# Optimization experiments

Measured on AMD Instinct MI355X. Metric: run time of the kernel, lower is better.

Reference implementation:

```python
import jax, jax.numpy as jnp
import numpy as np

PS = 4          # patch size
C = 3           # channels
VOCAB = 512
D = 256         # embed dim
PD = PS * PS * C  # 48 patch dim


def _gelu(x):
    return jax.nn.gelu(x, approximate=False)  # torch nn.GELU default = exact erf


def setup_inputs() -> dict:
    key = jax.random.key(0)
    ks = jax.random.split(key, 16)
    frames = jax.random.uniform(ks[0], (32, 256, 256, 3), jnp.float32) * 255.0

    def lin(kw, kb, fan_in, fan_out):
        bound = 1.0 / np.sqrt(fan_in)
        w = jax.random.uniform(kw, (fan_out, fan_in), jnp.float32, -bound, bound)
        b = jax.random.uniform(kb, (fan_out,), jnp.float32, -bound, bound)
        return w, b

    enc_w1, enc_b1 = lin(ks[1], ks[2], PD, D)
    enc_w2, enc_b2 = lin(ks[3], ks[4], D, D)
    enc_w3, enc_b3 = lin(ks[5], ks[6], D, D)
    dec_w1, dec_b1 = lin(ks[7], ks[8], D, D)
    dec_w2, dec_b2 = lin(ks[9], ks[10], D, D)
    dec_w3, dec_b3 = lin(ks[11], ks[12], D, PD)
    codebook = jax.random.normal(ks[13], (VOCAB, D), jnp.float32) * 0.1
    return {
        'frames': frames,
        'enc_w1': enc_w1, 'enc_b1': enc_b1,
        'enc_w2': enc_w2, 'enc_b2': enc_b2,
        'enc_w3': enc_w3, 'enc_b3': enc_b3,
        'codebook': codebook,
        'dec_w1': dec_w1, 'dec_b1': dec_b1,
        'dec_w2': dec_w2, 'dec_b2': dec_b2,
        'dec_w3': dec_w3, 'dec_b3': dec_b3,
    }


def _patchify(x):  # [B,H,W,C] -> [B, N, ps*ps*C]
    B, H, W, Ch = x.shape
    h, w = H // PS, W // PS
    x = x.reshape(B, h, PS, w, PS, Ch).transpose(0, 1, 3, 2, 4, 5)
    return x.reshape(B, h * w, PS * PS * Ch)


def _unpatchify(p):  # [B, N, ps*ps*C] -> [B,H,W,C]
    B, N, _ = p.shape
    h = w = int(np.sqrt(N))
    p = p.reshape(B, h, w, PS, PS, C).transpose(0, 1, 3, 2, 4, 5)
    return p.reshape(B, h * PS, w * PS, C)


def reference(frames, enc_w1, enc_b1, enc_w2, enc_b2, enc_w3, enc_b3,
              codebook, dec_w1, dec_b1, dec_w2, dec_b2, dec_w3, dec_b3):
    x = frames / 255.0 * 2.0 - 1.0
    patches = _patchify(x)  # [B,N,48]
    # encoder MLP
    z = _gelu(patches @ enc_w1.T + enc_b1)
    z = _gelu(z @ enc_w2.T + enc_b2)
    z_e = z @ enc_w3.T + enc_b3  # [B,N,D]
    # nearest-codebook lookup (squared L2; argmin equals cdist argmin)
    d2 = (jnp.sum(z_e * z_e, -1, keepdims=True)
          - 2.0 * jnp.einsum('bnd,vd->bnv', z_e, codebook)
          + jnp.sum(codebook * codebook, -1))  # [B,N,V]
    tokens = jnp.argmin(d2, axis=-1)  # [B,N] int
    z_q = codebook[tokens]  # [B,N,D]
    z_q_st = z_e + jax.lax.stop_gradient(z_q - z_e)
    # decoder MLP
    y = _gelu(z_q_st @ dec_w1.T + dec_b1)
    y = _gelu(y @ dec_w2.T + dec_b2)
    y = y @ dec_w3.T + dec_b3  # [B,N,48]
    recon = _unpatchify(y)
    target = frames / 255.0 * 2.0 - 1.0
    recon_loss = jnp.mean((recon - target) ** 2)
    commitment_loss = jnp.mean((z_e - jax.lax.stop_gradient(z_q)) ** 2)
    codebook_loss = jnp.mean((z_q - jax.lax.stop_gradient(z_e)) ** 2)
    return recon, tokens, recon_loss, commitment_loss, codebook_loss
```

## Files before the change

kernel.cpp:

```cpp
#include <hip/hip_runtime.h>
#include <hip/hip_bf16.h>
#include <math.h>
#include <float.h>
#include <limits.h>

#define T_ROWS 131072

typedef __attribute__((ext_vector_type(8))) short short8;
typedef __attribute__((ext_vector_type(4))) float f32x4;

__device__ __forceinline__ float gelu_f(float x){
    return 0.5f * x * (1.0f + erff(x * 0.7071067811865475f));
}
__device__ __forceinline__ float bf2f(ushort u){
    union { unsigned int i; float f; } v; v.i = ((unsigned int)u) << 16; return v.f;
}
__device__ __forceinline__ ushort f2bf(float f){
    union { float f; unsigned int i; } v; v.f = f;
    unsigned int i = v.i;
    unsigned int r = (i + 0x7fffu + ((i >> 16) & 1u)) >> 16;
    return (ushort)r;
}
__device__ __forceinline__ void split3(float x, ushort &u0, ushort &u1, ushort &u2){
    union { float f; unsigned int i; } v; v.f = x;
    u0 = (ushort)(v.i >> 16);
    union { unsigned int i; float f; } h0; h0.i = ((unsigned int)u0) << 16;
    float r = x - h0.f;
    union { float f; unsigned int i; } vr; vr.f = r;
    u1 = (ushort)(vr.i >> 16);
    union { unsigned int i; float f; } h1; h1.i = ((unsigned int)u1) << 16;
    float r2 = r - h1.f;
    union { float f; unsigned int i; } v2; v2.f = r2;
    u2 = (ushort)(v2.i >> 16);
}

__global__ __launch_bounds__(256) void prep_kernel(
    const float* __restrict__ w2, const float* __restrict__ w3,
    const float* __restrict__ d1, const float* __restrict__ d2,
    const float* __restrict__ w1, const float* __restrict__ b1,
    const float* __restrict__ cb,
    ushort* __restrict__ w2s0, ushort* __restrict__ w2s1, ushort* __restrict__ w2s2,
    ushort* __restrict__ w3s0, ushort* __restrict__ w3s1, ushort* __restrict__ w3s2,
    ushort* __restrict__ w1b, ushort* __restrict__ w2b,
    float* __restrict__ cn, ushort* __restrict__ cbb,
    ushort* __restrict__ cbs0, ushort* __restrict__ cbs1, ushort* __restrict__ cbs2,
    ushort* __restrict__ w1p0, ushort* __restrict__ w1p1, ushort* __restrict__ w1p2,
    float* __restrict__ bias2)
{
    const int blk = blockIdx.x, tid = threadIdx.x;
    if (blk < 64){
        const int i = (blk*256 + tid)*4;
        float4 a = *(const float4*)(w2 + i);
        ushort4 s0, s1, s2;
        split3(a.x, s0.x, s1.x, s2.x); split3(a.y, s0.y, s1.y, s2.y);
        split3(a.z, s0.z, s1.z, s2.z); split3(a.w, s0.w, s1.w, s2.w);
        *(ushort4*)(w2s0+i)=s0; *(ushort4*)(w2s1+i)=s1; *(ushort4*)(w2s2+i)=s2;
        float4 b = *(const float4*)(w3 + i);
        split3(b.x, s0.x, s1.x, s2.x); split3(b.y, s0.y, s1.y, s2.y);
        split3(b.z, s0.z, s1.z, s2.z); split3(b.w, s0.w, s1.w, s2.w);
        *(ushort4*)(w3s0+i)=s0; *(ushort4*)(w3s1+i)=s1; *(ushort4*)(w3s2+i)=s2;
        float4 c = *(const float4*)(d1 + i);
        ushort4 u; u.x=f2bf(c.x); u.y=f2bf(c.y); u.z=f2bf(c.z); u.w=f2bf(c.w);
        *(ushort4*)(w1b+i) = u;
        float4 d = *(const float4*)(d2 + i);
        u.x=f2bf(d.x); u.y=f2bf(d.y); u.z=f2bf(d.z); u.w=f2bf(d.w);
        *(ushort4*)(w2b+i) = u;
    } else if (blk < 192){
        const int lane = tid & 63;
        const int code = (blk-64)*4 + (tid >> 6);
        float4 v = ((const float4*)(cb + (size_t)code*256))[lane];
        size_t off = (size_t)code*256 + lane*4;
        ushort4 u; u.x=f2bf(v.x); u.y=f2bf(v.y); u.z=f2bf(v.z); u.w=f2bf(v.w);
        *(ushort4*)(cbb + off) = u;
        ushort4 s0, s1, s2;
        split3(v.x, s0.x, s1.x, s2.x); split3(v.y, s0.y, s1.y, s2.y);
        split3(v.z, s0.z, s1.z, s2.z); split3(v.w, s0.w, s1.w, s2.w);
        *(ushort4*)(cbs0 + off) = s0;
        *(ushort4*)(cbs1 + off) = s1;
        *(ushort4*)(cbs2 + off) = s2;
        float s = v.x*v.x + v.y*v.y + v.z*v.z + v.w*v.w;
        #pragma unroll
        for (int m=1; m<64; m<<=1) s += __shfl_xor(s, m);
        if (lane == 0) cn[code] = s;
    } else if (blk < 208){
        const int idx = (blk-192)*256 + tid;
        const int n = idx >> 4, k = (idx & 15)*4;
        ushort4 s0 = {0,0,0,0}, s1 = {0,0,0,0}, s2 = {0,0,0,0};
        if (k < 48){
            float4 v = *(const float4*)(w1 + n*48 + k);
            split3(v.x, s0.x, s1.x, s2.x); split3(v.y, s0.y, s1.y, s2.y);
            split3(v.z, s0.z, s1.z, s2.z); split3(v.w, s0.w, s1.w, s2.w);
        }
        *(ushort4*)(w1p0 + n*64 + k) = s0;
        *(ushort4*)(w1p1 + n*64 + k) = s1;
        *(ushort4*)(w1p2 + n*64 + k) = s2;
    } else {
        float s = 0.0f;
        for (int k=0;k<48;++k) s += w1[tid*48 + k];
        bias2[tid] = b1[tid] - s;
    }
}

template<int KTOT, bool GELU, int LOADER, bool SCALE>
__global__ __launch_bounds__(256, 3) void split6_gemm(
    const float* __restrict__ Ain,
    const float* __restrict__ frames,
    const ushort* __restrict__ W0, const ushort* __restrict__ W1,
    const ushort* __restrict__ W2,
    const float* __restrict__ bias,
    float* __restrict__ Cout)
{
    __shared__ __align__(16) ushort Al[3][64][40];
    __shared__ __align__(16) ushort Wl[256][40];

    const int tid = threadIdx.x;
    const int m0 = blockIdx.x * 64;
    const int arow = tid >> 2, q = tid & 3;
    const int lane = tid & 63;
    const int w = tid >> 6;
    const int lr = lane & 15, lg = lane >> 4;

    const float* asrc = nullptr;
    int pbase = 0;
    if constexpr (LOADER == 0){
        asrc = Ain + (size_t)(m0 + arow)*KTOT + q*8;
    } else {
        int p = m0 + arow;
        int b = p >> 12, nl = p & 4095, hh = nl >> 6, ww = nl & 63;
        pbase = ((b*256 + hh*4)*256 + ww*4)*3;
    }
    const ushort* wsrc  = W0 + (size_t)tid*KTOT;
    const ushort* w1frag = W1 + (size_t)(w*64 + lr)*KTOT + lg*8;
    const ushort* w2frag = W2 + (size_t)(w*64 + lr)*KTOT + lg*8;

    f32x4 acc[4][4];
    #pragma unroll
    for (int mi=0;mi<4;++mi)
        #pragma unroll
        for (int ni=0;ni<4;++ni)
            acc[mi][ni] = (f32x4){0.f,0.f,0.f,0.f};

    for (int k0=0; k0<KTOT; k0+=32){
        float x[8];
        if constexpr (LOADER == 0){
            *(float4*)&x[0] = *(const float4*)(asrc + k0);
            *(float4*)&x[4] = *(const float4*)(asrc + k0 + 4);
        } else {
            #pragma unroll
            for (int j=0;j<2;++j){
                int kk = k0 + q*8 + j*4;
                float4 v = {0.f,0.f,0.f,0.f};
                if (kk < 48){
                    int ph = kk/12, rem = kk - ph*12;
                    v = *(const float4*)(frames + pbase + ph*768 + rem);
                }
                x[j*4+0]=v.x; x[j*4+1]=v.y; x[j*4+2]=v.z; x[j*4+3]=v.w;
            }
        }
        ushort t0[8], t1[8], t2[8];
        #pragma unroll
        for (int e=0;e<8;++e) split3(x[e], t0[e], t1[e], t2[e]);
        *(uint4*)&Al[0][arow][q*8] = *(const uint4*)t0;
        *(uint4*)&Al[1][arow][q*8] = *(const uint4*)t1;
        *(uint4*)&Al[2][arow][q*8] = *(const uint4*)t2;
        *(uint4*)&Wl[tid][0]  = *(const uint4*)(wsrc + k0);
        *(uint4*)&Wl[tid][8]  = *(const uint4*)(wsrc + k0 + 8);
        *(uint4*)&Wl[tid][16] = *(const uint4*)(wsrc + k0 + 16);
        *(uint4*)&Wl[tid][24] = *(const uint4*)(wsrc + k0 + 24);
        short8 b1v[4], b2v[4];
        #pragma unroll
        for (int ni=0;ni<4;++ni){
            b1v[ni] = *(const short8*)(w1frag + (size_t)ni*16*KTOT + k0);
            b2v[ni] = *(const short8*)(w2frag + (size_t)ni*16*KTOT + k0);
        }
        __syncthreads();

        short8 b0v[4];
        #pragma unroll
        for (int ni=0;ni<4;++ni)
            b0v[ni] = *(const short8*)&Wl[w*64 + ni*16 + lr][lg*8];
        #pragma unroll
        for (int mi=0;mi<4;++mi){
            short8 a0 = *(const short8*)&Al[0][mi*16 + lr][lg*8];
            short8 a1 = *(const short8*)&Al[1][mi*16 + lr][lg*8];
            short8 a2 = *(const short8*)&Al[2][mi*16 + lr][lg*8];
            #pragma unroll
            for (int ni=0;ni<4;++ni)
                acc[mi][ni] = __builtin_amdgcn_mfma_f32_16x16x32_bf16(a0, b0v[ni], acc[mi][ni], 0,0,0);
            #pragma unroll
            for (int ni=0;ni<4;++ni)
                acc[mi][ni] = __builtin_amdgcn_mfma_f32_16x16x32_bf16(a0, b1v[ni], acc[mi][ni], 0,0,0);
            #pragma unroll
            for (int ni=0;ni<4;++ni)
                acc[mi][ni] = __builtin_amdgcn_mfma_f32_16x16x32_bf16(a1, b0v[ni], acc[mi][ni], 0,0,0);
            #pragma unroll
            for (int ni=0;ni<4;++ni)
                acc[mi][ni] = __builtin_amdgcn_mfma_f32_16x16x32_bf16(a0, b2v[ni], acc[mi][ni], 0,0,0);
            #pragma unroll
            for (int ni=0;ni<4;++ni)
                acc[mi][ni] = __builtin_amdgcn_mfma_f32_16x16x32_bf16(a1, b1v[ni], acc[mi][ni], 0,0,0);
            #pragma unroll
            for (int ni=0;ni<4;++ni)
                acc[mi][ni] = __builtin_amdgcn_mfma_f32_16x16x32_bf16(a2, b0v[ni], acc[mi][ni], 0,0,0);
        }
        __syncthreads();
    }

    const float alpha = 2.0f/255.0f;
    float bn[4];
    #pragma unroll
    for (int ni=0;ni<4;++ni) bn[ni] = bias[w*64 + ni*16 + lr];
    #pragma unroll
    for (int mi=0;mi<4;++mi)
        #pragma unroll
        for (int ni=0;ni<4;++ni)
            #pragma unroll
            for (int r=0;r<4;++r){
                int row = m0 + mi*16 + lg*4 + r;
                float v;
                if (SCALE) v = fmaf(alpha, acc[mi][ni][r], bn[ni]);
                else       v = acc[mi][ni][r] + bn[ni];
                if (GELU) v = gelu_f(v);
                Cout[(size_t)row*256 + w*64 + ni*16 + lr] = v;
            }
}

#define INSERT1(dv, iv) do { \
    float _d = (dv); int _i = (iv); \
    if (_d < bd || (_d == bd && _i < bi)){ bd = _d; bi = _i; } \
} while(0)

__global__ __launch_bounds__(256, 3) void tokens_split6(
    const float* __restrict__ Zf,
    const ushort* __restrict__ C0, const ushort* __restrict__ C1,
    const ushort* __restrict__ C2,
    const float* __restrict__ cn,
    float2* __restrict__ partials,
    float* __restrict__ zz_out)
{
    __shared__ __align__(16) ushort Al[3][128][40];
    __shared__ __align__(16) ushort Wl[2][128][40];
    __shared__ float2 ptop[128][2];

    const int tid = threadIdx.x;
    const int m0 = blockIdx.x * 128;
    const int n0 = blockIdx.y * 128;
    const int srow = tid >> 1, shalf = (tid & 1) * 16;
    const int lane = tid & 63;
    const int w = tid >> 6;
    const int wm = (w >> 1) * 64, wn = (w & 1) * 64;
    const int lr = lane & 15, lg = lane >> 4;

    const float*  asrc = Zf + (size_t)(m0 + srow)*256 + shalf;
    const ushort* ws0  = C0 + (size_t)(n0 + srow)*256 + shalf;
    const ushort* ws1  = C1 + (size_t)(n0 + srow)*256 + shalf;
    const ushort* c2frag = C2 + (size_t)(n0 + wn + lr)*256 + lg*8;

    f32x4 acc[4][4];
    #pragma unroll
    for (int mi=0;mi<4;++mi)
        #pragma unroll
        for (int ni=0;ni<4;++ni)
            acc[mi][ni] = (f32x4){0.f,0.f,0.f,0.f};

    float zzp = 0.0f;

    for (int k0=0; k0<256; k0+=32){
        float x[16];
        *(float4*)&x[0]  = *(const float4*)(asrc + k0);
        *(float4*)&x[4]  = *(const float4*)(asrc + k0 + 4);
        *(float4*)&x[8]  = *(const float4*)(asrc + k0 + 8);
        *(float4*)&x[12] = *(const float4*)(asrc + k0 + 12);
        ushort t0[16], t1[16], t2[16];
        #pragma unroll
        for (int e=0;e<16;++e){
            split3(x[e], t0[e], t1[e], t2[e]);
            zzp = fmaf(x[e], x[e], zzp);
        }
        *(uint4*)&Al[0][srow][shalf]   = *(const uint4*)&t0[0];
        *(uint4*)&Al[0][srow][shalf+8] = *(const uint4*)&t0[8];
        *(uint4*)&Al[1][srow][shalf]   = *(const uint4*)&t1[0];
        *(uint4*)&Al[1][srow][shalf+8] = *(const uint4*)&t1[8];
        *(uint4*)&Al[2][srow][shalf]   = *(const uint4*)&t2[0];
        *(uint4*)&Al[2][srow][shalf+8] = *(const uint4*)&t2[8];
        *(uint4*)&Wl[0][srow][shalf]   = *(const uint4*)(ws0 + k0);
        *(uint4*)&Wl[0][srow][shalf+8] = *(const uint4*)(ws0 + k0 + 8);
        *(uint4*)&Wl[1][srow][shalf]   = *(const uint4*)(ws1 + k0);
        *(uint4*)&Wl[1][srow][shalf+8] = *(const uint4*)(ws1 + k0 + 8);
        short8 b2[4];
        #pragma unroll
        for (int ni=0;ni<4;++ni)
            b2[ni] = *(const short8*)(c2frag + (size_t)ni*16*256 + k0);
        __syncthreads();

        short8 b0[4], b1[4];
        #pragma unroll
        for (int ni=0;ni<4;++ni){
            b0[ni] = *(const short8*)&Wl[0][wn + ni*16 + lr][lg*8];
            b1[ni] = *(const short8*)&Wl[1][wn + ni*16 + lr][lg*8];
        }
        #pragma unroll
        for (int mi=0;mi<4;++mi){
            short8 a0 = *(const short8*)&Al[0][wm + mi*16 + lr][lg*8];
            short8 a1 = *(const short8*)&Al[1][wm + mi*16 + lr][lg*8];
            short8 a2 = *(const short8*)&Al[2][wm + mi*16 + lr][lg*8];
            #pragma unroll
            for (int ni=0;ni<4;++ni)
                acc[mi][ni] = __builtin_amdgcn_mfma_f32_16x16x32_bf16(a0, b0[ni], acc[mi][ni], 0,0,0);
            #pragma unroll
            for (int ni=0;ni<4;++ni)
                acc[mi][ni] = __builtin_amdgcn_mfma_f32_16x16x32_bf16(a0, b1[ni], acc[mi][ni], 0,0,0);
            #pragma unroll
            for (int ni=0;ni<4;++ni)
                acc[mi][ni] = __builtin_amdgcn_mfma_f32_16x16x32_bf16(a1, b0[ni], acc[mi][ni], 0,0,0);
            #pragma unroll
            for (int ni=0;ni<4;++ni)
                acc[mi][ni] = __builtin_amdgcn_mfma_f32_16x16x32_bf16(a0, b2[ni], acc[mi][ni], 0,0,0);
            #pragma unroll
            for (int ni=0;ni<4;++ni)
                acc[mi][ni] = __builtin_amdgcn_mfma_f32_16x16x32_bf16(a1, b1[ni], acc[mi][ni], 0,0,0);
            #pragma unroll
            for (int ni=0;ni<4;++ni)
                acc[mi][ni] = __builtin_amdgcn_mfma_f32_16x16x32_bf16(a2, b0[ni], acc[mi][ni], 0,0,0);
        }
        __syncthreads();
    }

    {
        float other = __shfl_xor(zzp, 1);
        if (blockIdx.y == 0 && (tid & 1) == 0)
            zz_out[m0 + srow] = zzp + other;
    }

    float cnl[4];
    #pragma unroll
    for (int ni=0;ni<4;++ni) cnl[ni] = cn[n0 + wn + ni*16 + lr];

    #pragma unroll
    for (int mi=0;mi<4;++mi)
        #pragma unroll
        for (int r=0;r<4;++r){
            float bd = FLT_MAX; int bi = INT_MAX;
            #pragma unroll
            for (int ni=0;ni<4;++ni){
                float d = cnl[ni] - 2.0f*acc[mi][ni][r];
                int col = n0 + wn + ni*16 + lr;
                INSERT1(d, col);
            }
            #pragma unroll
            for (int m=1; m<16; m<<=1){
                float od = __shfl_xor(bd, m);
                int   oi = __shfl_xor(bi, m);
                INSERT1(od, oi);
            }
            if (lr == 0)
                ptop[wm + mi*16 + lg*4 + r][w & 1] = make_float2(bd, (float)bi);
        }
    __syncthreads();
    if (tid < 128){
        float2 hA = ptop[tid][0], hB = ptop[tid][1];
        int   gA = (int)hA.y, gB = (int)hB.y;
        bool takeB = (hB.x < hA.x) || (hB.x == hA.x && gB < gA);
        partials[(size_t)(m0 + tid)*4 + blockIdx.y] = takeB ? hB : hA;
    }
}

__global__ __launch_bounds__(256) void token_reduce(
    const float* __restrict__ zz_out, const float2* __restrict__ partials,
    float* __restrict__ tokf, float* __restrict__ loss)
{
    const int tid = threadIdx.x;
    const int row = blockIdx.x*256 + tid;
    float2 p0 = partials[(size_t)row*4 + 0];
    float2 p1 = partials[(size_t)row*4 + 1];
    float2 p2 = partials[(size_t)row*4 + 2];
    float2 p3 = partials[(size_t)row*4 + 3];
    float d = p0.x; int g = (int)p0.y;
    if (p1.x < d || (p1.x == d && (int)p1.y < g)){ d = p1.x; g = (int)p1.y; }
    if (p2.x < d || (p2.x == d && (int)p2.y < g)){ d = p2.x; g = (int)p2.y; }
    if (p3.x < d || (p3.x == d && (int)p3.y < g)){ d = p3.x; g = (int)p3.y; }
    tokf[row] = (float)g;
    float cs = zz_out[row] + d;
    #pragma unroll
    for (int m=1; m<64; m<<=1) cs += __shfl_xor(cs, m);
    __shared__ float wsum[4];
    const int lane = tid & 63, w = tid >> 6;
    if (lane == 0) wsum[w] = cs;
    __syncthreads();
    if (tid == 0) atomicAdd(loss + 1, wsum[0]+wsum[1]+wsum[2]+wsum[3]);
}

__global__ __launch_bounds__(256) void mfma_gemm(
    const ushort* __restrict__ Abf,
    const ushort* __restrict__ Wbf,
    const float* __restrict__ bias,
    ushort* __restrict__ Ybf)
{
    __shared__ __align__(16) ushort Al[128][40];
    __shared__ __align__(16) ushort Wl[128][40];

    const int tid = threadIdx.x;
    const int m0 = blockIdx.x * 128;
    const int n0 = blockIdx.y * 128;
    const int srow = tid >> 1, shalf = (tid & 1) * 16;
    const int lane = tid & 63;
    const int w = tid >> 6;
    const int wm = (w >> 1) * 64, wn = (w & 1) * 64;
    const int lr = lane & 15, lg = lane >> 4;

    const ushort* asrc = Abf + (size_t)(m0 + srow)*256 + shalf;
    const ushort* wsrc = Wbf + (size_t)(n0 + srow)*256 + shalf;

    f32x4 acc[4][4];
    #pragma unroll
    for (int mi=0;mi<4;++mi)
        #pragma unroll
        for (int ni=0;ni<4;++ni)
            acc[mi][ni] = (f32x4){0.f,0.f,0.f,0.f};

    for (int k0=0; k0<256; k0+=32){
        *(uint4*)&Al[srow][shalf]   = *(const uint4*)(asrc + k0);
        *(uint4*)&Al[srow][shalf+8] = *(const uint4*)(asrc + k0 + 8);
        *(uint4*)&Wl[srow][shalf]   = *(const uint4*)(wsrc + k0);
        *(uint4*)&Wl[srow][shalf+8] = *(const uint4*)(wsrc + k0 + 8);
        __syncthreads();

        short8 af[4], bfr[4];
        #pragma unroll
        for (int mi=0;mi<4;++mi)
            af[mi] = *(const short8*)&Al[wm + mi*16 + lr][lg*8];
        #pragma unroll
        for (int ni=0;ni<4;++ni)
            bfr[ni] = *(const short8*)&Wl[wn + ni*16 + lr][lg*8];
        #pragma unroll
        for (int mi=0;mi<4;++mi)
            #pragma unroll
            for (int ni=0;ni<4;++ni)
                acc[mi][ni] = __builtin_amdgcn_mfma_f32_16x16x32_bf16(
                    af[mi], bfr[ni], acc[mi][ni], 0, 0, 0);
        __syncthreads();
    }

    float bn[4];
    #pragma unroll
    for (int ni=0;ni<4;++ni) bn[ni] = bias[n0 + wn + ni*16 + lr];
    #pragma unroll
    for (int mi=0;mi<4;++mi)
        #pragma unroll
        for (int ni=0;ni<4;++ni)
            #pragma unroll
            for (int r=0;r<4;++r){
                int row = m0 + wm + mi*16 + lg*4 + r;
                float v = acc[mi][ni][r] + bn[ni];
                v = gelu_f(v);
                Ybf[(size_t)row*256 + n0 + wn + ni*16 + lr] = f2bf(v);
            }
}

__global__ __launch_bounds__(256) void dec3_table(
    const ushort* __restrict__ Ain, const float* __restrict__ W,
    const float* __restrict__ bias, float* __restrict__ Rt)
{
    __shared__ __align__(16) ushort Al[256][40];
    __shared__ __align__(16) ushort Wl[48][40];

    const int tid = threadIdx.x;
    const int m0 = blockIdx.x * 256;
    const int lane = tid & 63;
    const int w = tid >> 6;
    const int lr = lane & 15, lg = lane >> 4;

    const ushort* asrc = Ain + (size_t)(m0 + tid)*256;

    f32x4 acc[4][3];
    #pragma unroll
    for (int mi=0;mi<4;++mi)
        #pragma unroll
        for (int ni=0;ni<3;++ni)
            acc[mi][ni] = (f32x4){0.f,0.f,0.f,0.f};

    for (int k0=0; k0<256; k0+=32){
        *(uint4*)&Al[tid][0]  = *(const uint4*)(asrc + k0);
        *(uint4*)&Al[tid][8]  = *(const uint4*)(asrc + k0 + 8);
        *(uint4*)&Al[tid][16] = *(const uint4*)(asrc + k0 + 16);
        *(uint4*)&Al[tid][24] = *(const uint4*)(asrc + k0 + 24);
        if (tid < 96){
            const int wrow = tid >> 1, wh = (tid & 1)*16;
            const float* wp = W + (size_t)wrow*256 + k0 + wh;
            float4 f0 = *(const float4*)(wp);
            float4 f1 = *(const float4*)(wp+4);
            float4 f2 = *(const float4*)(wp+8);
            float4 f3 = *(const float4*)(wp+12);
            ushort t[16];
            t[0]=f2bf(f0.x); t[1]=f2bf(f0.y); t[2]=f2bf(f0.z); t[3]=f2bf(f0.w);
            t[4]=f2bf(f1.x); t[5]=f2bf(f1.y); t[6]=f2bf(f1.z); t[7]=f2bf(f1.w);
            t[8]=f2bf(f2.x); t[9]=f2bf(f2.y); t[10]=f2bf(f2.z); t[11]=f2bf(f2.w);
            t[12]=f2bf(f3.x); t[13]=f2bf(f3.y); t[14]=f2bf(f3.z); t[15]=f2bf(f3.w);
            *(uint4*)&Wl[wrow][wh]   = *(const uint4*)&t[0];
            *(uint4*)&Wl[wrow][wh+8] = *(const uint4*)&t[8];
        }
        __syncthreads();

        short8 bfr[3];
        #pragma unroll
        for (int ni=0;ni<3;++ni)
            bfr[ni] = *(const short8*)&Wl[ni*16 + lr][lg*8];
        #pragma unroll
        for (int mi=0;mi<4;++mi){
            short8 af = *(const short8*)&Al[w*64 + mi*16 + lr][lg*8];
            #pragma unroll
            for (int ni=0;ni<3;++ni)
                acc[mi][ni] = __builtin_amdgcn_mfma_f32_16x16x32_bf16(
                    af, bfr[ni], acc[mi][ni], 0, 0, 0);
        }
        __syncthreads();
    }

    #pragma unroll
    for (int ni=0;ni<3;++ni){
        const int col = ni*16 + lr;
        const float bn = bias[col];
        #pragma unroll
        for (int mi=0;mi<4;++mi)
            #pragma unroll
            for (int r=0;r<4;++r){
                int row = m0 + w*64 + mi*16 + lg*4 + r;
                Rt[row*48 + col] = acc[mi][ni][r] + bn;
            }
    }
}

__global__ __launch_bounds__(256) void gather_recon(
    const float* __restrict__ Rt, const float* __restrict__ tokf,
    const float* __restrict__ frames, float* __restrict__ recon,
    float* __restrict__ loss)
{
    const int tid = threadIdx.x;
    const int idx = blockIdx.x*256 + tid;
    const int p = idx >> 2, ph = idx & 3;
    const int g = (int)tokf[p];
    int b = p >> 12, nl = p & 4095, hh = nl >> 6, ww = nl & 63;
    size_t base = (size_t)(((b*256 + hh*4 + ph)*256 + ww*4)*3);
    const float* rp = Rt + g*48 + ph*12;
    const float sc = 2.0f/255.0f;
    float ls = 0.0f;
    #pragma unroll
    for (int j=0;j<3;++j){
        float4 y = *(const float4*)(rp + j*4);
        float4 f = *(const float4*)(frames + base + j*4);
        float t0=f.x*sc-1.0f, t1=f.y*sc-1.0f, t2=f.z*sc-1.0f, t3=f.w*sc-1.0f;
        float d0=y.x-t0, d1=y.y-t1, d2=y.z-t2, d3=y.w-t3;
        ls += d0*d0 + d1*d1 + d2*d2 + d3*d3;
        *(float4*)(recon + base + j*4) = y;
    }
    #pragma unroll
    for (int off=32; off>0; off>>=1) ls += __shfl_down(ls, off);
    __shared__ float wsum[4];
    int lane = tid & 63, w = tid >> 6;
    if (lane == 0) wsum[w] = ls;
    __syncthreads();
    if (tid == 0) atomicAdd(loss + 0, wsum[0]+wsum[1]+wsum[2]+wsum[3]);
}

__global__ void finalize_kernel(float* __restrict__ loss){
    if (threadIdx.x == 0 && blockIdx.x == 0){
        loss[0] = loss[0] * (1.0f/6291456.0f);
        float c = loss[1] * (1.0f/33554432.0f);
        loss[1] = c;
        loss[2] = c;
    }
}

extern "C" void kernel_launch(void* const* d_in, const int* in_sizes, int n_in,
                              void* d_out, int out_size, void* d_ws, size_t ws_size,
                              hipStream_t stream)
{
    (void)in_sizes; (void)n_in; (void)out_size; (void)ws_size;
    const float* frames   = (const float*)d_in[0];
    const float* enc_w1   = (const float*)d_in[1];
    const float* enc_b1   = (const float*)d_in[2];
    const float* enc_w2   = (const float*)d_in[3];
    const float* enc_b2   = (const float*)d_in[4];
    const float* enc_w3   = (const float*)d_in[5];
    const float* enc_b3   = (const float*)d_in[6];
    const float* codebook = (const float*)d_in[7];
    const float* dec_w1   = (const float*)d_in[8];
    const float* dec_b1   = (const float*)d_in[9];
    const float* dec_w2   = (const float*)d_in[10];
    const float* dec_b2   = (const float*)d_in[11];
    const float* dec_w3   = (const float*)d_in[12];
    const float* dec_b3   = (const float*)d_in[13];

    float* P = (float*)d_ws;
    float* Q = P + (size_t)33554432;
    float2* partials = (float2*)(Q + 18000000);
    ushort* L1 = (ushort*)P;
    ushort* L2 = (ushort*)(P + 65536);
    float*  Rt = P + 131072;

    float* recon = (float*)d_out;
    float* tokf  = recon + 6291456;
    float* loss  = tokf + 131072;
    float*  cn   = recon;
    ushort* cbb  = (ushort*)(recon + 512);
    ushort* w1b  = (ushort*)(recon + 66048);
    ushort* w2b  = (ushort*)(recon + 98816);
    ushort* w2s0 = (ushort*)(recon + 131584);
    ushort* w2s1 = (ushort*)(recon + 164352);
    ushort* w2s2 = (ushort*)(recon + 197120);
    ushort* w3s0 = (ushort*)(recon + 229888);
    ushort* w3s1 = (ushort*)(recon + 262656);
    ushort* w3s2 = (ushort*)(recon + 295424);
    ushort* cbs0 = (ushort*)(recon + 328192);
    ushort* cbs1 = (ushort*)(recon + 393728);
    ushort* cbs2 = (ushort*)(recon + 459264);
    float*  zzb  = recon + 524800;
    ushort* w1p0 = (ushort*)(recon + 655872);
    ushort* w1p1 = (ushort*)(recon + 664064);
    ushort* w1p2 = (ushort*)(recon + 672256);
    float*  bias2 = recon + 680448;

    hipMemsetAsync(loss, 0, 3*sizeof(float), stream);

    dim3 blk(256);
    prep_kernel<<<dim3(209), blk, 0, stream>>>(enc_w2, enc_w3, dec_w1, dec_w2,
        enc_w1, enc_b1, codebook,
        w2s0, w2s1, w2s2, w3s0, w3s1, w3s2, w1b, w2b,
        cn, cbb, cbs0, cbs1, cbs2, w1p0, w1p1, w1p2, bias2);
    split6_gemm<64,  true, 1, true ><<<dim3(T_ROWS/64), blk, 0, stream>>>(nullptr, frames, w1p0, w1p1, w1p2, bias2, P);
    split6_gemm<256, true, 0, false><<<dim3(T_ROWS/64), blk, 0, stream>>>(P, nullptr, w2s0, w2s1, w2s2, enc_b2, Q);
    split6_gemm<256, false,0, false><<<dim3(T_ROWS/64), blk, 0, stream>>>(Q, nullptr, w3s0, w3s1, w3s2, enc_b3, P);
    tokens_split6<<<dim3(T_ROWS/128, 4), blk, 0, stream>>>(P, cbs0, cbs1, cbs2, cn, partials, zzb);
    token_reduce<<<dim3(T_ROWS/256), blk, 0, stream>>>(zzb, partials, tokf, loss);
    mfma_gemm<<<dim3(4, 2), blk, 0, stream>>>(cbb, w1b, dec_b1, L1);
    mfma_gemm<<<dim3(4, 2), blk, 0, stream>>>(L1, w2b, dec_b2, L2);
    dec3_table<<<dim3(2), blk, 0, stream>>>(L2, dec_w3, dec_b3, Rt);
    gather_recon<<<dim3(T_ROWS*4/256), blk, 0, stream>>>(Rt, tokf, frames, recon, loss);
    finalize_kernel<<<dim3(1), dim3(64), 0, stream>>>(loss);
}
```

Measured before the change: 597.7 us.

## Emit pre-split bf16 z_e and row norms from enc3 GEMM epilogue for token search

The third encoder GEMM now writes z_e directly as three bf16 split planes and computes per-row squared norms in its epilogue. A new token-search kernel reads those planes instead of re-splitting fp32 z_e in each of the four codebook column blocks. This removes repeated split work and the fp32 reads in the token kernel. In exchange it writes three ushort planes (same byte count as fp32 times 1.5) and needs a larger workspace, with fallback to the old path if the workspace is too small.

```diff
diff --git a/kernel.cpp b/kernel.cpp
--- a/kernel.cpp
+++ b/kernel.cpp
@@ -225,6 +225,117 @@
             }
 }
 
+__global__ __launch_bounds__(256, 3) void split6_zout(
+    const float* __restrict__ Ain,
+    const ushort* __restrict__ W0, const ushort* __restrict__ W1,
+    const ushort* __restrict__ W2,
+    const float* __restrict__ bias,
+    ushort* __restrict__ zb0, ushort* __restrict__ zb1, ushort* __restrict__ zb2,
+    float* __restrict__ zz_out)
+{
+    __shared__ __align__(16) ushort Al[3][64][40];
+    __shared__ __align__(16) ushort Wl[256][40];
+    __shared__ float zs[64][4];
+
+    const int tid = threadIdx.x;
+    const int m0 = blockIdx.x * 64;
+    const int arow = tid >> 2, q = tid & 3;
+    const int lane = tid & 63;
+    const int w = tid >> 6;
+    const int lr = lane & 15, lg = lane >> 4;
+
+    const float* asrc = Ain + (size_t)(m0 + arow)*256 + q*8;
+    const ushort* wsrc  = W0 + (size_t)tid*256;
+    const ushort* w1frag = W1 + (size_t)(w*64 + lr)*256 + lg*8;
+    const ushort* w2frag = W2 + (size_t)(w*64 + lr)*256 + lg*8;
+
+    f32x4 acc[4][4];
+    #pragma unroll
+    for (int mi=0;mi<4;++mi)
+        #pragma unroll
+        for (int ni=0;ni<4;++ni)
+            acc[mi][ni] = (f32x4){0.f,0.f,0.f,0.f};
+
+    for (int k0=0; k0<256; k0+=32){
+        float x[8];
+        *(float4*)&x[0] = *(const float4*)(asrc + k0);
+        *(float4*)&x[4] = *(const float4*)(asrc + k0 + 4);
+        ushort t0[8], t1[8], t2[8];
+        #pragma unroll
+        for (int e=0;e<8;++e) split3(x[e], t0[e], t1[e], t2[e]);
+        *(uint4*)&Al[0][arow][q*8] = *(const uint4*)t0;
+        *(uint4*)&Al[1][arow][q*8] = *(const uint4*)t1;
+        *(uint4*)&Al[2][arow][q*8] = *(const uint4*)t2;
+        *(uint4*)&Wl[tid][0]  = *(const uint4*)(wsrc + k0);
+        *(uint4*)&Wl[tid][8]  = *(const uint4*)(wsrc + k0 + 8);
+        *(uint4*)&Wl[tid][16] = *(const uint4*)(wsrc + k0 + 16);
+        *(uint4*)&Wl[tid][24] = *(const uint4*)(wsrc + k0 + 24);
+        short8 b1v[4], b2v[4];
+        #pragma unroll
+        for (int ni=0;ni<4;++ni){
+            b1v[ni] = *(const short8*)(w1frag + (size_t)ni*16*256 + k0);
+            b2v[ni] = *(const short8*)(w2frag + (size_t)ni*16*256 + k0);
+        }
+        __syncthreads();
+
+        short8 b0v[4];
+        #pragma unroll
+        for (int ni=0;ni<4;++ni)
+            b0v[ni] = *(const short8*)&Wl[w*64 + ni*16 + lr][lg*8];
+        #pragma unroll
+        for (int mi=0;mi<4;++mi){
+            short8 a0 = *(const short8*)&Al[0][mi*16 + lr][lg*8];
+            short8 a1 = *(const short8*)&Al[1][mi*16 + lr][lg*8];
+            short8 a2 = *(const short8*)&Al[2][mi*16 + lr][lg*8];
+            #pragma unroll
+            for (int ni=0;ni<4;++ni)
+                acc[mi][ni] = __builtin_amdgcn_mfma_f32_16x16x32_bf16(a0, b0v[ni], acc[mi][ni], 0,0,0);
+            #pragma unroll
+            for (int ni=0;ni<4;++ni)
+                acc[mi][ni] = __builtin_amdgcn_mfma_f32_16x16x32_bf16(a0, b1v[ni], acc[mi][ni], 0,0,0);
+            #pragma unroll
+            for (int ni=0;ni<4;++ni)
+                acc[mi][ni] = __builtin_amdgcn_mfma_f32_16x16x32_bf16(a1, b0v[ni], acc[mi][ni], 0,0,0);
+            #pragma unroll
+            for (int ni=0;ni<4;++ni)
+                acc[mi][ni] = __builtin_amdgcn_mfma_f32_16x16x32_bf16(a0, b2v[ni], acc[mi][ni], 0,0,0);
+            #pragma unroll
+            for (int ni=0;ni<4;++ni)
+                acc[mi][ni] = __builtin_amdgcn_mfma_f32_16x16x32_bf16(a1, b1v[ni], acc[mi][ni], 0,0,0);
+            #pragma unroll
+            for (int ni=0;ni<4;++ni)
+                acc[mi][ni] = __builtin_amdgcn_mfma_f32_16x16x32_bf16(a2, b0v[ni], acc[mi][ni], 0,0,0);
+        }
+        __syncthreads();
+    }
+
+    float bn[4];
+    #pragma unroll
+    for (int ni=0;ni<4;++ni) bn[ni] = bias[w*64 + ni*16 + lr];
+    #pragma unroll
+    for (int mi=0;mi<4;++mi)
+        #pragma unroll
+        for (int r=0;r<4;++r){
+            int row = m0 + mi*16 + lg*4 + r;
+            float p = 0.0f;
+            #pragma unroll
+            for (int ni=0;ni<4;++ni){
+                float v = acc[mi][ni][r] + bn[ni];
+                p = fmaf(v, v, p);
+                ushort s0, s1, s2;
+                split3(v, s0, s1, s2);
+                size_t off = (size_t)row*256 + w*64 + ni*16 + lr;
+                zb0[off] = s0; zb1[off] = s1; zb2[off] = s2;
+            }
+            p += __shfl_xor(p, 1); p += __shfl_xor(p, 2);
+            p += __shfl_xor(p, 4); p += __shfl_xor(p, 8);
+            if (lr == 0) zs[mi*16 + lg*4 + r][w] = p;
+        }
+    __syncthreads();
+    if (tid < 64)
+        zz_out[m0 + tid] = zs[tid][0] + zs[tid][1] + zs[tid][2] + zs[tid][3];
+}
+
 #define INSERT1(dv, iv) do { \
     float _d = (dv); int _i = (iv); \
     if (_d < bd || (_d == bd && _i < bi)){ bd = _d; bi = _i; } \
@@ -330,6 +441,122 @@
         float other = __shfl_xor(zzp, 1);
         if (blockIdx.y == 0 && (tid & 1) == 0)
             zz_out[m0 + srow] = zzp + other;
+    }
+
+    float cnl[4];
+    #pragma unroll
+    for (int ni=0;ni<4;++ni) cnl[ni] = cn[n0 + wn + ni*16 + lr];
+
+    #pragma unroll
+    for (int mi=0;mi<4;++mi)
+        #pragma unroll
+        for (int r=0;r<4;++r){
+            float bd = FLT_MAX; int bi = INT_MAX;
+            #pragma unroll
+            for (int ni=0;ni<4;++ni){
+                float d = cnl[ni] - 2.0f*acc[mi][ni][r];
+                int col = n0 + wn + ni*16 + lr;
+                INSERT1(d, col);
+            }
+            #pragma unroll
+            for (int m=1; m<16; m<<=1){
+                float od = __shfl_xor(bd, m);
+                int   oi = __shfl_xor(bi, m);
+                INSERT1(od, oi);
+            }
+            if (lr == 0)
+                ptop[wm + mi*16 + lg*4 + r][w & 1] = make_float2(bd, (float)bi);
+        }
+    __syncthreads();
+    if (tid < 128){
+        float2 hA = ptop[tid][0], hB = ptop[tid][1];
+        int   gA = (int)hA.y, gB = (int)hB.y;
+        bool takeB = (hB.x < hA.x) || (hB.x == hA.x && gB < gA);
+        partials[(size_t)(m0 + tid)*4 + blockIdx.y] = takeB ? hB : hA;
+    }
+}
+
+__global__ __launch_bounds__(256, 3) void tokens_split6_pp(
+    const ushort* __restrict__ Z0, const ushort* __restrict__ Z1,
+    const ushort* __restrict__ Z2,
+    const ushort* __restrict__ C0, const ushort* __restrict__ C1,
+    const ushort* __restrict__ C2,
+    const float* __restrict__ cn,
+    float2* __restrict__ partials)
+{
+    __shared__ __align__(16) ushort Al[3][128][40];
+    __shared__ __align__(16) ushort Wl[2][128][40];
+    __shared__ float2 ptop[128][2];
+
+    const int tid = threadIdx.x;
+    const int m0 = blockIdx.x * 128;
+    const int n0 = blockIdx.y * 128;
+    const int srow = tid >> 1, shalf = (tid & 1) * 16;
+    const int lane = tid & 63;
+    const int w = tid >> 6;
+    const int wm = (w >> 1) * 64, wn = (w & 1) * 64;
+    const int lr = lane & 15, lg = lane >> 4;
+
+    const size_t arow_off = (size_t)(m0 + srow)*256 + shalf;
+    const ushort* ws0  = C0 + (size_t)(n0 + srow)*256 + shalf;
+    const ushort* ws1  = C1 + (size_t)(n0 + srow)*256 + shalf;
+    const ushort* c2frag = C2 + (size_t)(n0 + wn + lr)*256 + lg*8;
+
+    f32x4 acc[4][4];
+    #pragma unroll
+    for (int mi=0;mi<4;++mi)
+        #pragma unroll
+        for (int ni=0;ni<4;++ni)
+            acc[mi][ni] = (f32x4){0.f,0.f,0.f,0.f};
+
+    for (int k0=0; k0<256; k0+=32){
+        *(uint4*)&Al[0][srow][shalf]   = *(const uint4*)(Z0 + arow_off + k0);
+        *(uint4*)&Al[0][srow][shalf+8] = *(const uint4*)(Z0 + arow_off + k0 + 8);
+        *(uint4*)&Al[1][srow][shalf]   = *(const uint4*)(Z1 + arow_off + k0);
+        *(uint4*)&Al[1][srow][shalf+8] = *(const uint4*)(Z1 + arow_off + k0 + 8);
+        *(uint4*)&Al[2][srow][shalf]   = *(const uint4*)(Z2 + arow_off + k0);
+        *(uint4*)&Al[2][srow][shalf+8] = *(const uint4*)(Z2 + arow_off + k0 + 8);
+        *(uint4*)&Wl[0][srow][shalf]   = *(const uint4*)(ws0 + k0);
+        *(uint4*)&Wl[0][srow][shalf+8] = *(const uint4*)(ws0 + k0 + 8);
+        *(uint4*)&Wl[1][srow][shalf]   = *(const uint4*)(ws1 + k0);
+        *(uint4*)&Wl[1][srow][shalf+8] = *(const uint4*)(ws1 + k0 + 8);
+        short8 b2[4];
+        #pragma unroll
+        for (int ni=0;ni<4;++ni)
+            b2[ni] = *(const short8*)(c2frag + (size_t)ni*16*256 + k0);
+        __syncthreads();
+
+        short8 b0[4], b1[4];
+        #pragma unroll
+        for (int ni=0;ni<4;++ni){
+            b0[ni] = *(const short8*)&Wl[0][wn + ni*16 + lr][lg*8];
+            b1[ni] = *(const short8*)&Wl[1][wn + ni*16 + lr][lg*8];
+        }
+        #pragma unroll
+        for (int mi=0;mi<4;++mi){
+            short8 a0 = *(const short8*)&Al[0][wm + mi*16 + lr][lg*8];
+            short8 a1 = *(const short8*)&Al[1][wm + mi*16 + lr][lg*8];
+            short8 a2 = *(const short8*)&Al[2][wm + mi*16 + lr][lg*8];
+            #pragma unroll
+            for (int ni=0;ni<4;++ni)
+                acc[mi][ni] = __builtin_amdgcn_mfma_f32_16x16x32_bf16(a0, b0[ni], acc[mi][ni], 0,0,0);
+            #pragma unroll
+            for (int ni=0;ni<4;++ni)
+                acc[mi][ni] = __builtin_amdgcn_mfma_f32_16x16x32_bf16(a0, b1[ni], acc[mi][ni], 0,0,0);
+            #pragma unroll
+            for (int ni=0;ni<4;++ni)
+                acc[mi][ni] = __builtin_amdgcn_mfma_f32_16x16x32_bf16(a1, b0[ni], acc[mi][ni], 0,0,0);
+            #pragma unroll
+            for (int ni=0;ni<4;++ni)
+                acc[mi][ni] = __builtin_amdgcn_mfma_f32_16x16x32_bf16(a0, b2[ni], acc[mi][ni], 0,0,0);
+            #pragma unroll
+            for (int ni=0;ni<4;++ni)
+                acc[mi][ni] = __builtin_amdgcn_mfma_f32_16x16x32_bf16(a1, b1[ni], acc[mi][ni], 0,0,0);
+            #pragma unroll
+            for (int ni=0;ni<4;++ni)
+                acc[mi][ni] = __builtin_amdgcn_mfma_f32_16x16x32_bf16(a2, b0[ni], acc[mi][ni], 0,0,0);
+        }
+        __syncthreads();
     }
 
     float cnl[4];
@@ -575,7 +802,7 @@
                               void* d_out, int out_size, void* d_ws, size_t ws_size,
                               hipStream_t stream)
 {
-    (void)in_sizes; (void)n_in; (void)out_size; (void)ws_size;
+    (void)in_sizes; (void)n_in; (void)out_size;
     const float* frames   = (const float*)d_in[0];
     const float* enc_w1   = (const float*)d_in[1];
     const float* enc_b1   = (const float*)d_in[2];
@@ -597,6 +824,12 @@
     ushort* L1 = (ushort*)P;
     ushort* L2 = (ushort*)(P + 65536);
     float*  Rt = P + 131072;
+    const size_t basefloats = (size_t)2*33554432;
+    ushort* zb0 = (ushort*)(P + basefloats);
+    ushort* zb1 = zb0 + (size_t)T_ROWS*256;
+    ushort* zb2 = zb1 + (size_t)T_ROWS*256;
+    const size_t need = basefloats*4 + (size_t)3*T_ROWS*256*2;
+    const bool big_ws = (ws_size >= need);
 
     float* recon = (float*)d_out;
     float* tokf  = recon + 6291456;
@@ -629,8 +862,13 @@
         cn, cbb, cbs0, cbs1, cbs2, w1p0, w1p1, w1p2, bias2);
     split6_gemm<64,  true, 1, true ><<<dim3(T_ROWS/64), blk, 0, stream>>>(nullptr, frames, w1p0, w1p1, w1p2, bias2, P);
     split6_gemm<256, true, 0, false><<<dim3(T_ROWS/64), blk, 0, stream>>>(P, nullptr, w2s0, w2s1, w2s2, enc_b2, Q);
-    split6_gemm<256, false,0, false><<<dim3(T_ROWS/64), blk, 0, stream>>>(Q, nullptr, w3s0, w3s1, w3s2, enc_b3, P);
-    tokens_split6<<<dim3(T_ROWS/128, 4), blk, 0, stream>>>(P, cbs0, cbs1, cbs2, cn, partials, zzb);
+    if (big_ws){
+        split6_zout<<<dim3(T_ROWS/64), blk, 0, stream>>>(Q, w3s0, w3s1, w3s2, enc_b3, zb0, zb1, zb2, zzb);
+        tokens_split6_pp<<<dim3(T_ROWS/128, 4), blk, 0, stream>>>(zb0, zb1, zb2, cbs0, cbs1, cbs2, cn, partials);
+    } else {
+        split6_gemm<256, false,0, false><<<dim3(T_ROWS/64), blk, 0, stream>>>(Q, nullptr, w3s0, w3s1, w3s2, enc_b3, P);
+        tokens_split6<<<dim3(T_ROWS/128, 4), blk, 0, stream>>>(P, cbs0, cbs1, cbs2, cn, partials, zzb);
+    }
     token_reduce<<<dim3(T_ROWS/256), blk, 0, stream>>>(zzb, partials, tokf, loss);
     mfma_gemm<<<dim3(4, 2), blk, 0, stream>>>(cbb, w1b, dec_b1, L1);
     mfma_gemm<<<dim3(4, 2), blk, 0, stream>>>(L1, w2b, dec_b2, L2);
```

After: 597.6 us. Within noise of the previous version (-0.0%).

## Emit pre-split bf16 z_e from encoder layer 3 and process tokens in halves

Applied to the files above, without the earlier changes.

Adds a dedicated encoder-layer-3 kernel that writes z_e directly as three bf16 split planes and computes the row squared norms. The token-search kernel then loads the pre-split planes instead of reloading fp32 z_e and re-splitting it in each of its four column blocks. The work runs in two row halves so the split buffers fit in workspace and can stay cache-resident between producer and consumer. The cost is more launches and three ushort planes written and read in place of one fp32 tensor.

```diff
diff --git a/kernel.cpp b/kernel.cpp
--- a/kernel.cpp
+++ b/kernel.cpp
@@ -5,15 +5,13 @@
 #include <limits.h>
 
 #define T_ROWS 131072
+#define HROWS  65536
 
 typedef __attribute__((ext_vector_type(8))) short short8;
 typedef __attribute__((ext_vector_type(4))) float f32x4;
 
 __device__ __forceinline__ float gelu_f(float x){
     return 0.5f * x * (1.0f + erff(x * 0.7071067811865475f));
-}
-__device__ __forceinline__ float bf2f(ushort u){
-    union { unsigned int i; float f; } v; v.i = ((unsigned int)u) << 16; return v.f;
 }
 __device__ __forceinline__ ushort f2bf(float f){
     union { float f; unsigned int i; } v; v.f = f;
@@ -225,18 +223,129 @@
             }
 }
 
+__global__ __launch_bounds__(256, 3) void split6_zout(
+    const float* __restrict__ Ain,
+    const ushort* __restrict__ W0, const ushort* __restrict__ W1,
+    const ushort* __restrict__ W2,
+    const float* __restrict__ bias,
+    ushort* __restrict__ zb0, ushort* __restrict__ zb1, ushort* __restrict__ zb2,
+    float* __restrict__ zz_out)
+{
+    __shared__ __align__(16) ushort Al[3][64][40];
+    __shared__ __align__(16) ushort Wl[256][40];
+    __shared__ float zs[64][4];
+
+    const int tid = threadIdx.x;
+    const int m0 = blockIdx.x * 64;
+    const int arow = tid >> 2, q = tid & 3;
+    const int lane = tid & 63;
+    const int w = tid >> 6;
+    const int lr = lane & 15, lg = lane >> 4;
+
+    const float* asrc = Ain + (size_t)(m0 + arow)*256 + q*8;
+    const ushort* wsrc  = W0 + (size_t)tid*256;
+    const ushort* w1frag = W1 + (size_t)(w*64 + lr)*256 + lg*8;
+    const ushort* w2frag = W2 + (size_t)(w*64 + lr)*256 + lg*8;
+
+    f32x4 acc[4][4];
+    #pragma unroll
+    for (int mi=0;mi<4;++mi)
+        #pragma unroll
+        for (int ni=0;ni<4;++ni)
+            acc[mi][ni] = (f32x4){0.f,0.f,0.f,0.f};
+
+    for (int k0=0; k0<256; k0+=32){
+        float x[8];
+        *(float4*)&x[0] = *(const float4*)(asrc + k0);
+        *(float4*)&x[4] = *(const float4*)(asrc + k0 + 4);
+        ushort t0[8], t1[8], t2[8];
+        #pragma unroll
+        for (int e=0;e<8;++e) split3(x[e], t0[e], t1[e], t2[e]);
+        *(uint4*)&Al[0][arow][q*8] = *(const uint4*)t0;
+        *(uint4*)&Al[1][arow][q*8] = *(const uint4*)t1;
+        *(uint4*)&Al[2][arow][q*8] = *(const uint4*)t2;
+        *(uint4*)&Wl[tid][0]  = *(const uint4*)(wsrc + k0);
+        *(uint4*)&Wl[tid][8]  = *(const uint4*)(wsrc + k0 + 8);
+        *(uint4*)&Wl[tid][16] = *(const uint4*)(wsrc + k0 + 16);
+        *(uint4*)&Wl[tid][24] = *(const uint4*)(wsrc + k0 + 24);
+        short8 b1v[4], b2v[4];
+        #pragma unroll
+        for (int ni=0;ni<4;++ni){
+            b1v[ni] = *(const short8*)(w1frag + (size_t)ni*16*256 + k0);
+            b2v[ni] = *(const short8*)(w2frag + (size_t)ni*16*256 + k0);
+        }
+        __syncthreads();
+
+        short8 b0v[4];
+        #pragma unroll
+        for (int ni=0;ni<4;++ni)
+            b0v[ni] = *(const short8*)&Wl[w*64 + ni*16 + lr][lg*8];
+        #pragma unroll
+        for (int mi=0;mi<4;++mi){
+            short8 a0 = *(const short8*)&Al[0][mi*16 + lr][lg*8];
+            short8 a1 = *(const short8*)&Al[1][mi*16 + lr][lg*8];
+            short8 a2 = *(const short8*)&Al[2][mi*16 + lr][lg*8];
+            #pragma unroll
+            for (int ni=0;ni<4;++ni)
+                acc[mi][ni] = __builtin_amdgcn_mfma_f32_16x16x32_bf16(a0, b0v[ni], acc[mi][ni], 0,0,0);
+            #pragma unroll
+            for (int ni=0;ni<4;++ni)
+                acc[mi][ni] = __builtin_amdgcn_mfma_f32_16x16x32_bf16(a0, b1v[ni], acc[mi][ni], 0,0,0);
+            #pragma unroll
+            for (int ni=0;ni<4;++ni)
+                acc[mi][ni] = __builtin_amdgcn_mfma_f32_16x16x32_bf16(a1, b0v[ni], acc[mi][ni], 0,0,0);
+            #pragma unroll
+            for (int ni=0;ni<4;++ni)
+                acc[mi][ni] = __builtin_amdgcn_mfma_f32_16x16x32_bf16(a0, b2v[ni], acc[mi][ni], 0,0,0);
+            #pragma unroll
+            for (int ni=0;ni<4;++ni)
+                acc[mi][ni] = __builtin_amdgcn_mfma_f32_16x16x32_bf16(a1, b1v[ni], acc[mi][ni], 0,0,0);
+            #pragma unroll
+            for (int ni=0;ni<4;++ni)
+                acc[mi][ni] = __builtin_amdgcn_mfma_f32_16x16x32_bf16(a2, b0v[ni], acc[mi][ni], 0,0,0);
+        }
+        __syncthreads();
+    }
+
+    float bn[4];
+    #pragma unroll
+    for (int ni=0;ni<4;++ni) bn[ni] = bias[w*64 + ni*16 + lr];
+    #pragma unroll
+    for (int mi=0;mi<4;++mi)
+        #pragma unroll
+        for (int r=0;r<4;++r){
+            int row = m0 + mi*16 + lg*4 + r;
+            float p = 0.0f;
+            #pragma unroll
+            for (int ni=0;ni<4;++ni){
+                float v = acc[mi][ni][r] + bn[ni];
+                p = fmaf(v, v, p);
+                ushort s0, s1, s2;
+                split3(v, s0, s1, s2);
+                size_t off = (size_t)row*256 + w*64 + ni*16 + lr;
+                zb0[off] = s0; zb1[off] = s1; zb2[off] = s2;
+            }
+            p += __shfl_xor(p, 1); p += __shfl_xor(p, 2);
+            p += __shfl_xor(p, 4); p += __shfl_xor(p, 8);
+            if (lr == 0) zs[mi*16 + lg*4 + r][w] = p;
+        }
+    __syncthreads();
+    if (tid < 64)
+        zz_out[m0 + tid] = zs[tid][0] + zs[tid][1] + zs[tid][2] + zs[tid][3];
+}
+
 #define INSERT1(dv, iv) do { \
     float _d = (dv); int _i = (iv); \
     if (_d < bd || (_d == bd && _i < bi)){ bd = _d; bi = _i; } \
 } while(0)
 
-__global__ __launch_bounds__(256, 3) void tokens_split6(
-    const float* __restrict__ Zf,
+__global__ __launch_bounds__(256, 3) void tokens_split6_pp(
+    const ushort* __restrict__ Z0, const ushort* __restrict__ Z1,
+    const ushort* __restrict__ Z2,
     const ushort* __restrict__ C0, const ushort* __restrict__ C1,
     const ushort* __restrict__ C2,
     const float* __restrict__ cn,
-    float2* __restrict__ partials,
-    float* __restrict__ zz_out)
+    float2* __restrict__ partials)
 {
     __shared__ __align__(16) ushort Al[3][128][40];
     __shared__ __align__(16) ushort Wl[2][128][40];
@@ -251,7 +360,7 @@
     const int wm = (w >> 1) * 64, wn = (w & 1) * 64;
     const int lr = lane & 15, lg = lane >> 4;
 
-    const float*  asrc = Zf + (size_t)(m0 + srow)*256 + shalf;
+    const size_t arow_off = (size_t)(m0 + srow)*256 + shalf;
     const ushort* ws0  = C0 + (size_t)(n0 + srow)*256 + shalf;
     const ushort* ws1  = C1 + (size_t)(n0 + srow)*256 + shalf;
     const ushort* c2frag = C2 + (size_t)(n0 + wn + lr)*256 + lg*8;
@@ -263,26 +372,13 @@
         for (int ni=0;ni<4;++ni)
             acc[mi][ni] = (f32x4){0.f,0.f,0.f,0.f};
 
-    float zzp = 0.0f;
-
     for (int k0=0; k0<256; k0+=32){
-        float x[16];
-        *(float4*)&x[0]  = *(const float4*)(asrc + k0);
-        *(float4*)&x[4]  = *(const float4*)(asrc + k0 + 4);
-        *(float4*)&x[8]  = *(const float4*)(asrc + k0 + 8);
-        *(float4*)&x[12] = *(const float4*)(asrc + k0 + 12);
-        ushort t0[16], t1[16], t2[16];
-        #pragma unroll
-        for (int e=0;e<16;++e){
-            split3(x[e], t0[e], t1[e], t2[e]);
-            zzp = fmaf(x[e], x[e], zzp);
-        }
-        *(uint4*)&Al[0][srow][shalf]   = *(const uint4*)&t0[0];
-        *(uint4*)&Al[0][srow][shalf+8] = *(const uint4*)&t0[8];
-        *(uint4*)&Al[1][srow][shalf]   = *(const uint4*)&t1[0];
-        *(uint4*)&Al[1][srow][shalf+8] = *(const uint4*)&t1[8];
-        *(uint4*)&Al[2][srow][shalf]   = *(const uint4*)&t2[0];
-        *(uint4*)&Al[2][srow][shalf+8] = *(const uint4*)&t2[8];
+        *(uint4*)&Al[0][srow][shalf]   = *(const uint4*)(Z0 + arow_off + k0);
+        *(uint4*)&Al[0][srow][shalf+8] = *(const uint4*)(Z0 + arow_off + k0 + 8);
+        *(uint4*)&Al[1][srow][shalf]   = *(const uint4*)(Z1 + arow_off + k0);
+        *(uint4*)&Al[1][srow][shalf+8] = *(const uint4*)(Z1 + arow_off + k0 + 8);
+        *(uint4*)&Al[2][srow][shalf]   = *(const uint4*)(Z2 + arow_off + k0);
+        *(uint4*)&Al[2][srow][shalf+8] = *(const uint4*)(Z2 + arow_off + k0 + 8);
         *(uint4*)&Wl[0][srow][shalf]   = *(const uint4*)(ws0 + k0);
         *(uint4*)&Wl[0][srow][shalf+8] = *(const uint4*)(ws0 + k0 + 8);
         *(uint4*)&Wl[1][srow][shalf]   = *(const uint4*)(ws1 + k0);
@@ -324,12 +420,6 @@
                 acc[mi][ni] = __builtin_amdgcn_mfma_f32_16x16x32_bf16(a2, b0[ni], acc[mi][ni], 0,0,0);
         }
         __syncthreads();
-    }
-
-    {
-        float other = __shfl_xor(zzp, 1);
-        if (blockIdx.y == 0 && (tid & 1) == 0)
-            zz_out[m0 + srow] = zzp + other;
     }
 
     float cnl[4];
@@ -593,7 +683,9 @@
 
     float* P = (float*)d_ws;
     float* Q = P + (size_t)33554432;
-    float2* partials = (float2*)(Q + 18000000);
+    ushort* zb0 = (ushort*)P;
+    ushort* zb1 = zb0 + (size_t)HROWS*256;
+    ushort* zb2 = zb1 + (size_t)HROWS*256;
     ushort* L1 = (ushort*)P;
     ushort* L2 = (ushort*)(P + 65536);
     float*  Rt = P + 131072;
@@ -619,6 +711,7 @@
     ushort* w1p1 = (ushort*)(recon + 664064);
     ushort* w1p2 = (ushort*)(recon + 672256);
     float*  bias2 = recon + 680448;
+    float2* partials = (float2*)(recon + 700416);
 
     hipMemsetAsync(loss, 0, 3*sizeof(float), stream);
 
@@ -629,8 +722,13 @@
         cn, cbb, cbs0, cbs1, cbs2, w1p0, w1p1, w1p2, bias2);
     split6_gemm<64,  true, 1, true ><<<dim3(T_ROWS/64), blk, 0, stream>>>(nullptr, frames, w1p0, w1p1, w1p2, bias2, P);
     split6_gemm<256, true, 0, false><<<dim3(T_ROWS/64), blk, 0, stream>>>(P, nullptr, w2s0, w2s1, w2s2, enc_b2, Q);
-    split6_gemm<256, false,0, false><<<dim3(T_ROWS/64), blk, 0, stream>>>(Q, nullptr, w3s0, w3s1, w3s2, enc_b3, P);
-    tokens_split6<<<dim3(T_ROWS/128, 4), blk, 0, stream>>>(P, cbs0, cbs1, cbs2, cn, partials, zzb);
+    for (int h = 0; h < 2; ++h){
+        const size_t roff = (size_t)h * HROWS;
+        split6_zout<<<dim3(HROWS/64), blk, 0, stream>>>(
+            Q + roff*256, w3s0, w3s1, w3s2, enc_b3, zb0, zb1, zb2, zzb + roff);
+        tokens_split6_pp<<<dim3(HROWS/128, 4), blk, 0, stream>>>(
+            zb0, zb1, zb2, cbs0, cbs1, cbs2, cn, partials + roff*4);
+    }
     token_reduce<<<dim3(T_ROWS/256), blk, 0, stream>>>(zzb, partials, tokf, loss);
     mfma_gemm<<<dim3(4, 2), blk, 0, stream>>>(cbb, w1b, dec_b1, L1);
     mfma_gemm<<<dim3(4, 2), blk, 0, stream>>>(L1, w2b, dec_b2, L2);
```

Result: slower. 709.9 us (+18.8%).
